# Performance work log

Measured on AMD Instinct MI355X. Metric: run time of the kernel, lower is better.

Reference implementation:

```python
import jax, jax.numpy as jnp
import numpy as np

DIM = 512
FEAT = 64
BATCH = 2048

def setup_inputs() -> dict:
    key = jax.random.key(0)
    kx, kw, kb = jax.random.split(key, 3)
    x = jax.random.normal(kx, (BATCH, DIM, FEAT), dtype=jnp.float32)
    # torch Linear weight is [out, in]; emulate Kaiming-uniform-ish init scale
    bound = 1.0 / np.sqrt(FEAT)
    W = jax.random.uniform(kw, (DIM, FEAT, FEAT), dtype=jnp.float32, minval=-bound, maxval=bound)
    b = jax.random.uniform(kb, (DIM, FEAT), dtype=jnp.float32, minval=-bound, maxval=bound)
    return {"x": x, "W": W, "b": b}

def reference(x, W, b):
    # per-slice Linear: out[:, d, :] = x[:, d, :] @ W[d].T + b[d]
    # fused as one batched contraction over the feature (input) axis 'f'
    return jnp.einsum('bdf,dgf->bdg', x, W) + b[None, :, :]
```

## Files before the change

kernel.cpp:

```cpp
#include <hip/hip_runtime.h>
#include <hip/hip_bf16.h>

#define DIM  512
#define FEAT 64
#define BATCH 2048

#define ROWS_PER_BLOCK 1024
#define TILES_PER_WAVE 16

using bf16x8 = __attribute__((ext_vector_type(8))) short;
using f32x4  = __attribute__((ext_vector_type(4))) float;

typedef __attribute__((address_space(3))) float lds_f;
typedef __attribute__((address_space(1))) const float glb_f;

__device__ inline short f2bf(float f) {
    unsigned int u = __float_as_uint(f);
    u += 0x7fffu + ((u >> 16) & 1u);
    return (short)(u >> 16);
}

__device__ inline bf16x8 cvt8(float4 a, float4 b) {
    bf16x8 r;
    r[0] = f2bf(a.x); r[1] = f2bf(a.y); r[2] = f2bf(a.z); r[3] = f2bf(a.w);
    r[4] = f2bf(b.x); r[5] = f2bf(b.y); r[6] = f2bf(b.z); r[7] = f2bf(b.w);
    return r;
}

__global__ __launch_bounds__(256, 3)
void split_linear_kernel(const float* __restrict__ x,
                         const float* __restrict__ W,
                         const float* __restrict__ bias,
                         float* __restrict__ out)
{
    __shared__ float xlds[4][2][1024];
    __shared__ float blds[FEAT];

    const int id    = blockIdx.x;
    const int xcd   = id & 7;
    const int chunk = id >> 3;
    const int nid   = xcd * 128 + chunk;
    const int d     = nid & (DIM - 1);
    const int b0    = (nid >> 9) * ROWS_PER_BLOCK;

    const int tid  = threadIdx.x;
    const int wave = tid >> 6;
    const int lane = tid & 63;
    const int lr   = lane & 15;
    const int lk   = lane >> 4;

    if (tid < FEAT) blds[tid] = bias[(size_t)d * FEAT + tid];
    __syncthreads();

    bf16x8 wf[2][4];
#pragma unroll
    for (int mt = 0; mt < 4; ++mt) {
        const float* wrow = W + ((size_t)d * FEAT + mt * 16 + lr) * FEAT + lk * 8;
#pragma unroll
        for (int ks = 0; ks < 2; ++ks) {
            float4 w0 = *(const float4*)(wrow + ks * 32);
            float4 w1 = *(const float4*)(wrow + ks * 32 + 4);
            wf[ks][mt] = cvt8(w0, w1);
        }
    }

    auto stage = [&](int slot, int tt) {
#pragma unroll
        for (int i = 0; i < 4; ++i) {
            const int r = i * 4 + (lane >> 4);
            const int c = (lane & 15) ^ (r & 7);
            const float* gp = x + ((size_t)(b0 + tt * 16 + r) * DIM + d) * FEAT + c * 4;
            __builtin_amdgcn_global_load_lds((glb_f*)gp,
                                             (lds_f*)&xlds[wave][slot][i * 256],
                                             16, 0, 0);
        }
    };

    stage(0, wave);
    stage(1, 4 + wave);

    for (int t = 0; t < TILES_PER_WAVE; ++t) {
        const int s = t & 1;
        if (t == 0 || t == TILES_PER_WAVE - 1)
            asm volatile("s_waitcnt vmcnt(4)" ::: "memory");
        else
            asm volatile("s_waitcnt vmcnt(8)" ::: "memory");
        __builtin_amdgcn_sched_barrier(0);

        float* sl = &xlds[wave][s][0];
        float4 p0a = *(const float4*)&sl[lr * 64 + (((lk * 2 + 0) ^ (lr & 7)) << 2)];
        float4 p0b = *(const float4*)&sl[lr * 64 + (((lk * 2 + 1) ^ (lr & 7)) << 2)];
        float4 p1a = *(const float4*)&sl[lr * 64 + (((8 + lk * 2 + 0) ^ (lr & 7)) << 2)];
        float4 p1b = *(const float4*)&sl[lr * 64 + (((8 + lk * 2 + 1) ^ (lr & 7)) << 2)];

        bf16x8 af0 = cvt8(p0a, p0b);
        bf16x8 af1 = cvt8(p1a, p1b);

        f32x4 acc[4];
#pragma unroll
        for (int mt = 0; mt < 4; ++mt)
            acc[mt] = *(const f32x4*)&blds[mt * 16 + lk * 4];
#pragma unroll
        for (int mt = 0; mt < 4; ++mt)
            acc[mt] = __builtin_amdgcn_mfma_f32_16x16x32_bf16(wf[0][mt], af0, acc[mt], 0, 0, 0);
#pragma unroll
        for (int mt = 0; mt < 4; ++mt)
            acc[mt] = __builtin_amdgcn_mfma_f32_16x16x32_bf16(wf[1][mt], af1, acc[mt], 0, 0, 0);

#pragma unroll
        for (int mt = 0; mt < 4; ++mt) {
            const int c  = mt * 4 + lk;
            const int pc = c ^ (lr & 7);
            *(f32x4*)&sl[lr * 64 + pc * 4] = acc[mt];
        }

        const int orow0 = b0 + (t * 4 + wave) * 16;
#pragma unroll
        for (int j = 0; j < 4; ++j) {
            const int rr  = j * 4 + (lane >> 4);
            const int cc  = lane & 15;
            const int pc2 = cc ^ (rr & 7);
            f32x4 v = *(const f32x4*)&sl[rr * 64 + pc2 * 4];
            __builtin_nontemporal_store(v,
                (f32x4*)(out + ((size_t)(orow0 + rr) * DIM + d) * FEAT + cc * 4));
        }
        __builtin_amdgcn_sched_barrier(0);

        if (t + 2 < TILES_PER_WAVE)
            stage(s, (t + 2) * 4 + wave);
    }
}

extern "C" void kernel_launch(void* const* d_in, const int* in_sizes, int n_in,
                              void* d_out, int out_size, void* d_ws, size_t ws_size,
                              hipStream_t stream) {
    const float* x    = (const float*)d_in[0];
    const float* W    = (const float*)d_in[1];
    const float* bias = (const float*)d_in[2];
    float* out        = (float*)d_out;

    dim3 grid(DIM * (BATCH / ROWS_PER_BLOCK), 1, 1);
    dim3 block(256, 1, 1);
    split_linear_kernel<<<grid, block, 0, stream>>>(x, W, bias, out);
}
```

Measured before the change: 104.0 us.

## Assign four adjacent slices per block, one per wave, with lockstep rows

Each block now covers four neighbouring d slices, one per wave, over 256 batch rows, instead of one slice over 1024 rows split across waves. A per-iteration s_barrier keeps the waves in lockstep, so at any moment a block reads and writes contiguous 1 KB row segments across the four slices rather than isolated 256-byte pieces. The aim is better DRAM and cache locality for the streamed x and out traffic. In exchange, each W slice is now fetched by eight blocks instead of two, and every tile iteration pays a workgroup barrier.

```diff
diff --git a/kernel.cpp b/kernel.cpp
--- a/kernel.cpp
+++ b/kernel.cpp
@@ -5,8 +5,8 @@
 #define FEAT 64
 #define BATCH 2048
 
-#define ROWS_PER_BLOCK 1024
-#define TILES_PER_WAVE 16
+#define ROWS_PER_BLOCK 256
+#define TILES 16
 
 using bf16x8 = __attribute__((ext_vector_type(8))) short;
 using f32x4  = __attribute__((ext_vector_type(4))) float;
@@ -34,23 +34,24 @@
                          float* __restrict__ out)
 {
     __shared__ float xlds[4][2][1024];
-    __shared__ float blds[FEAT];
+    __shared__ float blds[4][FEAT];
 
     const int id    = blockIdx.x;
     const int xcd   = id & 7;
     const int chunk = id >> 3;
     const int nid   = xcd * 128 + chunk;
-    const int d     = nid & (DIM - 1);
-    const int b0    = (nid >> 9) * ROWS_PER_BLOCK;
+    const int dg    = nid & 127;
+    const int rc    = nid >> 7;
+    const int b0    = rc * ROWS_PER_BLOCK;
 
     const int tid  = threadIdx.x;
     const int wave = tid >> 6;
     const int lane = tid & 63;
     const int lr   = lane & 15;
     const int lk   = lane >> 4;
+    const int d    = dg * 4 + wave;
 
-    if (tid < FEAT) blds[tid] = bias[(size_t)d * FEAT + tid];
-    __syncthreads();
+    blds[wave][lane] = bias[(size_t)d * FEAT + lane];
 
     bf16x8 wf[2][4];
 #pragma unroll
@@ -76,12 +77,13 @@
         }
     };
 
-    stage(0, wave);
-    stage(1, 4 + wave);
+    stage(0, 0);
+    stage(1, 1);
 
-    for (int t = 0; t < TILES_PER_WAVE; ++t) {
+    for (int t = 0; t < TILES; ++t) {
         const int s = t & 1;
-        if (t == 0 || t == TILES_PER_WAVE - 1)
+        __builtin_amdgcn_s_barrier();
+        if (t == 0 || t == TILES - 1)
             asm volatile("s_waitcnt vmcnt(4)" ::: "memory");
         else
             asm volatile("s_waitcnt vmcnt(8)" ::: "memory");
@@ -99,7 +101,7 @@
         f32x4 acc[4];
 #pragma unroll
         for (int mt = 0; mt < 4; ++mt)
-            acc[mt] = *(const f32x4*)&blds[mt * 16 + lk * 4];
+            acc[mt] = *(const f32x4*)&blds[wave][mt * 16 + lk * 4];
 #pragma unroll
         for (int mt = 0; mt < 4; ++mt)
             acc[mt] = __builtin_amdgcn_mfma_f32_16x16x32_bf16(wf[0][mt], af0, acc[mt], 0, 0, 0);
@@ -114,7 +116,7 @@
             *(f32x4*)&sl[lr * 64 + pc * 4] = acc[mt];
         }
 
-        const int orow0 = b0 + (t * 4 + wave) * 16;
+        const int orow0 = b0 + t * 16;
 #pragma unroll
         for (int j = 0; j < 4; ++j) {
             const int rr  = j * 4 + (lane >> 4);
@@ -126,8 +128,8 @@
         }
         __builtin_amdgcn_sched_barrier(0);
 
-        if (t + 2 < TILES_PER_WAVE)
-            stage(s, (t + 2) * 4 + wave);
+        if (t + 2 < TILES)
+            stage(s, t + 2);
     }
 }
 
@@ -139,7 +141,7 @@
     const float* bias = (const float*)d_in[2];
     float* out        = (float*)d_out;
 
-    dim3 grid(DIM * (BATCH / ROWS_PER_BLOCK), 1, 1);
+    dim3 grid((DIM / 4) * (BATCH / ROWS_PER_BLOCK), 1, 1);
     dim3 block(256, 1, 1);
     split_linear_kernel<<<grid, block, 0, stream>>>(x, W, bias, out);
 }
```

After: 107.4 us. 1.03x slower.
